# Performance work log

Hardware: AMD Instinct MI355X
Metric: run time of the kernel (lower is better)

## Reference

```python
import jax, jax.numpy as jnp
import numpy as np

B, S, D, H = 4, 2048, 1024, 16
HD = D // H

def rotate_half(x):
    x1, x2 = jnp.split(x, 2, axis=-1)
    return jnp.concatenate((-x2, x1), axis=-1)

def apply_rope(x, cos, sin):
    # x: [B,H,S,hd]; cos/sin: [S,hd] -> broadcast over B,H
    return x * cos[None, None] + rotate_half(x) * sin[None, None]

def setup_inputs() -> dict:
    key = jax.random.key(0)
    ks = jax.random.split(key, 8)
    x = jax.random.normal(ks[0], (B, S, D), dtype=jnp.float32)
    mask = jnp.triu(jnp.ones((S, S), dtype=bool), k=1)  # True = masked (causal)
    pos = jnp.arange(S, dtype=jnp.float32)[:, None]
    inv = 1.0 / (10000.0 ** (jnp.arange(0, HD, 2, dtype=jnp.float32) / HD))
    ang = pos * inv[None, :]  # [S, hd/2]
    ang = jnp.concatenate([ang, ang], axis=-1)  # [S, hd]
    rope_cos = jnp.cos(ang)
    rope_sin = jnp.sin(ang)
    scale = 1.0 / np.sqrt(D)
    Wq = jax.random.normal(ks[1], (D, D), dtype=jnp.float32) * scale
    Wk = jax.random.normal(ks[2], (D, D), dtype=jnp.float32) * scale
    Wv = jax.random.normal(ks[3], (D, D), dtype=jnp.float32) * scale
    Wo = jax.random.normal(ks[4], (D, D), dtype=jnp.float32) * scale
    z = jnp.zeros((D,), dtype=jnp.float32)
    return {"x": x, "mask": mask, "rope_cos": rope_cos, "rope_sin": rope_sin,
            "Wq": Wq, "bq": z, "Wk": Wk, "bk": z, "Wv": Wv, "bv": z, "Wo": Wo, "bo": z}

def reference(x, mask, rope_cos, rope_sin, Wq, bq, Wk, bk, Wv, bv, Wo, bo):
    b, s, d = x.shape
    def proj(W, bias):
        y = x @ W.T + bias  # torch Linear: x W^T + b
        return y.reshape(b, s, H, HD).transpose(0, 2, 1, 3)  # [B,H,S,hd]
    Q = apply_rope(proj(Wq, bq), rope_cos, rope_sin)
    K = apply_rope(proj(Wk, bk), rope_cos, rope_sin)
    V = proj(Wv, bv)
    scores = jnp.einsum('bhqd,bhkd->bhqk', Q, K) / jnp.sqrt(jnp.float32(HD))
    scores = jnp.where(mask[None, None], -jnp.inf, scores)
    attn = jax.nn.softmax(scores, axis=-1)
    ctx = jnp.einsum('bhqk,bhkd->bhqd', attn, V)
    ctx = ctx.transpose(0, 2, 1, 3).reshape(b, s, d)
    return ctx @ Wo.T + bo
```

## Files before the change

kernel.cpp:

```cpp
#include <hip/hip_runtime.h>
#include <hip/hip_bf16.h>

#define S_LEN 2048
#define D_MODEL 1024
#define NH 16
#define HDIM 64
#define B_SZ 4

typedef __attribute__((ext_vector_type(8))) short bf16x8;
typedef __attribute__((ext_vector_type(4))) float f32x4;

__device__ inline void gld16(const __hip_bfloat16* g, __hip_bfloat16* l) {
    __builtin_amdgcn_global_load_lds(
        (const __attribute__((address_space(1))) unsigned int*)g,
        (__attribute__((address_space(3))) unsigned int*)l, 16, 0, 0);
}

__device__ inline unsigned int pkbf(float a, float b) {
    float2 f; f.x = a; f.y = b;
    __hip_bfloat162 h = __float22bfloat162_rn(f);
    union { __hip_bfloat162 h; unsigned int u; } cv; cv.h = h; return cv.u;
}

__global__ __launch_bounds__(256) void f2bf4_kernel(const float4* __restrict__ in,
                                                    __hip_bfloat162* __restrict__ out,
                                                    int n4) {
    int i = blockIdx.x * 256 + threadIdx.x;
    if (i < n4) {
        float4 v = in[i];
        __hip_bfloat162 a, b;
        a.x = __float2bfloat16(v.x); a.y = __float2bfloat16(v.y);
        b.x = __float2bfloat16(v.z); b.y = __float2bfloat16(v.w);
        out[2 * i]     = a;
        out[2 * i + 1] = b;
    }
}

__global__ __launch_bounds__(256) void f2bfw_kernel(
    const float4* __restrict__ w0, const float4* __restrict__ w1,
    const float4* __restrict__ w2, const float4* __restrict__ w3,
    __hip_bfloat162* __restrict__ o0, __hip_bfloat162* __restrict__ o1,
    __hip_bfloat162* __restrict__ o2, __hip_bfloat162* __restrict__ o3) {
    const int z = blockIdx.y;
    const float4* in = (z == 0) ? w0 : (z == 1) ? w1 : (z == 2) ? w2 : w3;
    __hip_bfloat162* out = (z == 0) ? o0 : (z == 1) ? o1 : (z == 2) ? o2 : o3;
    int i = blockIdx.x * 256 + threadIdx.x;
    float4 v = in[i];
    __hip_bfloat162 a, b;
    a.x = __float2bfloat16(v.x); a.y = __float2bfloat16(v.y);
    b.x = __float2bfloat16(v.z); b.y = __float2bfloat16(v.w);
    out[2 * i]     = a;
    out[2 * i + 1] = b;
}

__device__ inline void gemm_mainloop(const __hip_bfloat16* __restrict__ X,
                                     const __hip_bfloat16* __restrict__ W,
                                     __hip_bfloat16* As, __hip_bfloat16* Bs,
                                     int m0, int n0, f32x4 acc[4][4]) {
    const int tid = threadIdx.x;
    const int wv = tid >> 6, lane = tid & 63, l15 = lane & 15, quad = lane >> 4;
    const int rw = (wv >> 1) * 64, cw = (wv & 1) * 64;
    for (int k0 = 0; k0 < D_MODEL; k0 += 32) {
        __syncthreads();
#pragma unroll
        for (int i = 0; i < 2; i++) {
            int l = tid + 256 * i;
            int row = l >> 2, c8 = (l & 3) * 8;
            gld16(&X[(size_t)(m0 + row) * D_MODEL + k0 + c8], &As[row * 32 + c8]);
            gld16(&W[(size_t)(n0 + row) * D_MODEL + k0 + c8], &Bs[row * 32 + c8]);
        }
        __syncthreads();
        bf16x8 af[4], bfr[4];
#pragma unroll
        for (int t = 0; t < 4; t++)
            af[t] = *(const bf16x8*)&As[(rw + t * 16 + l15) * 32 + quad * 8];
#pragma unroll
        for (int t = 0; t < 4; t++)
            bfr[t] = *(const bf16x8*)&Bs[(cw + t * 16 + l15) * 32 + quad * 8];
#pragma unroll
        for (int mt = 0; mt < 4; mt++)
#pragma unroll
            for (int nt = 0; nt < 4; nt++)
                acc[mt][nt] = __builtin_amdgcn_mfma_f32_16x16x32_bf16(
                    af[mt], bfr[nt], acc[mt][nt], 0, 0, 0);
    }
}

#define PT 136
__global__ __launch_bounds__(256) void qkv_kernel(
    const __hip_bfloat16* __restrict__ X,
    const __hip_bfloat16* __restrict__ W0, const __hip_bfloat16* __restrict__ W1,
    const __hip_bfloat16* __restrict__ W2,
    const float* __restrict__ b0, const float* __restrict__ b1,
    const float* __restrict__ b2,
    const float* __restrict__ rc, const float* __restrict__ rs,
    __hip_bfloat16* __restrict__ Qo, __hip_bfloat16* __restrict__ Ko,
    __hip_bfloat16* __restrict__ Vo) {
    __shared__ __hip_bfloat16 pool[64 * PT];
    __hip_bfloat16* As = pool;
    __hip_bfloat16* Bs = pool + 4096;
    const int z = blockIdx.z;
    const __hip_bfloat16* W = (z == 0) ? W0 : ((z == 1) ? W1 : W2);
    const float* bias = (z == 0) ? b0 : ((z == 1) ? b1 : b2);
    f32x4 acc[4][4];
#pragma unroll
    for (int i = 0; i < 4; i++)
#pragma unroll
        for (int j = 0; j < 4; j++) acc[i][j] = (f32x4){0.f, 0.f, 0.f, 0.f};
    const int m0 = blockIdx.x * 128, n0 = blockIdx.y * 128;
    gemm_mainloop(X, W, As, Bs, m0, n0, acc);

    const int tid = threadIdx.x;
    const int wv = tid >> 6, lane = tid & 63, l15 = lane & 15, quad = lane >> 4;
    const int rw = (wv >> 1) * 64, cw = (wv & 1) * 64;

    if (z == 2) {
        __hip_bfloat16* T = pool;
        const int b = m0 >> 11, s0l = m0 & (S_LEN - 1);
#pragma unroll
        for (int hn = 0; hn < 2; hn++) {
            __syncthreads();
            if ((wv & 1) == hn) {
#pragma unroll
                for (int mt = 0; mt < 4; mt++)
#pragma unroll
                    for (int nt = 0; nt < 4; nt++)
#pragma unroll
                        for (int r = 0; r < 4; r++) {
                            int dl = nt * 16 + l15;
                            int ml = rw + mt * 16 + quad * 4 + r;
                            T[dl * PT + ml] =
                                __float2bfloat16(acc[mt][nt][r] + bias[n0 + hn * 64 + dl]);
                        }
            }
            __syncthreads();
            const int d = tid >> 2, sc = tid & 3;
            const int h = (n0 >> 6) + hn;
            size_t gb = ((size_t)((b * NH + h) * HDIM + d)) * S_LEN + s0l + sc * 32;
#pragma unroll
            for (int j = 0; j < 4; j++) {
                bf16x8 v = *(const bf16x8*)&T[d * PT + sc * 32 + j * 8];
                *(bf16x8*)&Vo[gb + j * 8] = v;
            }
        }
    } else {
        __hip_bfloat16* dst = (z == 0) ? Qo : Ko;
        const float qs = (z == 0) ? 0.18033688011112042f : 1.0f;
#pragma unroll
        for (int mt = 0; mt < 4; mt++)
#pragma unroll
            for (int r = 0; r < 4; r++) {
                int m = m0 + rw + mt * 16 + quad * 4 + r;
                int s = m & (S_LEN - 1), b = m >> 11;
#pragma unroll
                for (int nt = 0; nt < 2; nt++) {
                    int n1 = n0 + cw + nt * 16 + l15;
                    int h = n1 >> 6, hd1 = n1 & 63;
                    float y1 = acc[mt][nt][r] + bias[n1];
                    float y2 = acc[mt][nt + 2][r] + bias[n1 + 32];
                    float c1 = rc[s * HDIM + hd1], s1 = rs[s * HDIM + hd1];
                    float c2 = rc[s * HDIM + hd1 + 32], s2 = rs[s * HDIM + hd1 + 32];
                    size_t base = (((size_t)(b * NH + h)) * S_LEN + s) * HDIM;
                    dst[base + hd1]      = __float2bfloat16((y1 * c1 - y2 * s1) * qs);
                    dst[base + hd1 + 32] = __float2bfloat16((y2 * c2 + y1 * s2) * qs);
                }
            }
    }
}

#define SWZ(r, c) (((r) << 6) + ((c) ^ (((r) & 7) << 3)))
__global__ __launch_bounds__(256) void attn_kernel(
    const __hip_bfloat16* __restrict__ Q, const __hip_bfloat16* __restrict__ K,
    const __hip_bfloat16* __restrict__ VT, __hip_bfloat16* __restrict__ CTX) {
    __shared__ __hip_bfloat16 Kl[2][64 * 64];
    __shared__ __hip_bfloat16 Vl[2][64 * 64];
    __shared__ __hip_bfloat16 Pl[2][4][16 * 64];
    const int tid = threadIdx.x;
    const int wv = tid >> 6, lane = tid & 63, l15 = lane & 15, quad = lane >> 4;
    const int bh = blockIdx.x;
    const int pr = blockIdx.y;
    const int tA = pr, tC = 31 - pr;
    const int nkb = tC + 1;
    const size_t off = (size_t)bh * S_LEN * HDIM;
    const __hip_bfloat16* Qp = Q + off;
    const __hip_bfloat16* Kp = K + off;
    const __hip_bfloat16* Vp = VT + off;
    __hip_bfloat16* PC = &Pl[0][wv][0];
    __hip_bfloat16* PA = &Pl[1][wv][0];

    const int e0 = wv * 512 + lane * 8;
    const int r0 = e0 >> 6, c80 = e0 & 63;
    const int sw0 = c80 ^ ((r0 & 7) << 3);
    const int r1 = r0 + 32;
    const int sw1 = c80 ^ ((r1 & 7) << 3);
    const __hip_bfloat16* ks0 = Kp + r0 * 64 + sw0;
    const __hip_bfloat16* ks1 = Kp + r1 * 64 + sw1;
    const __hip_bfloat16* vs0 = Vp + (size_t)r0 * S_LEN + sw0;
    const __hip_bfloat16* vs1 = Vp + (size_t)r1 * S_LEN + sw1;

    auto stage = [&](int kb, int bsel) {
        const int ko = kb * 64;
        gld16(ks0 + (size_t)ko * 64, &Kl[bsel][e0]);
        gld16(ks1 + (size_t)ko * 64, &Kl[bsel][e0 + 2048]);
        gld16(vs0 + ko, &Vl[bsel][e0]);
        gld16(vs1 + ko, &Vl[bsel][e0 + 2048]);
    };

    bf16x8 qfA[2], qfC[2];
#pragma unroll
    for (int c = 0; c < 2; c++) {
        qfA[c] = *(const bf16x8*)&Qp[(size_t)(tA * 64 + wv * 16 + l15) * HDIM + c * 32 + quad * 8];
        qfC[c] = *(const bf16x8*)&Qp[(size_t)(tC * 64 + wv * 16 + l15) * HDIM + c * 32 + quad * 8];
    }

    float lA = 0.f, lC = 0.f;
    f32x4 accA[4], accC[4];
#pragma unroll
    for (int nt = 0; nt < 4; nt++) {
        accA[nt] = (f32x4){0.f, 0.f, 0.f, 0.f};
        accC[nt] = (f32x4){0.f, 0.f, 0.f, 0.f};
    }

    const int qrel = wv * 16 + l15;

    stage(0, 0);
    __syncthreads();
    for (int kb = 0; kb < nkb; kb++) {
        const int buf = kb & 1;
        if (kb + 1 < nkb) stage(kb + 1, buf ^ 1);
        const __hip_bfloat16* Kb_ = &Kl[buf][0];
        const __hip_bfloat16* Vb_ = &Vl[buf][0];

        const bool aAct = (kb <= tA);
        unsigned int pkC[8], pkA[8];

        f32x4 saC[4], saA[4];
#pragma unroll
        for (int st = 0; st < 4; st++) {
            saC[st] = (f32x4){0.f, 0.f, 0.f, 0.f};
            saA[st] = (f32x4){0.f, 0.f, 0.f, 0.f};
        }
        __builtin_amdgcn_s_setprio(1);
        if (aAct) {
#pragma unroll
            for (int c = 0; c < 2; c++)
#pragma unroll
                for (int st = 0; st < 4; st++) {
                    bf16x8 kf = *(const bf16x8*)&Kb_[SWZ(st * 16 + l15, c * 32 + quad * 8)];
                    saC[st] = __builtin_amdgcn_mfma_f32_16x16x32_bf16(kf, qfC[c], saC[st], 0, 0, 0);
                    saA[st] = __builtin_amdgcn_mfma_f32_16x16x32_bf16(kf, qfA[c], saA[st], 0, 0, 0);
                }
        } else {
#pragma unroll
            for (int c = 0; c < 2; c++)
#pragma unroll
                for (int st = 0; st < 4; st++) {
                    bf16x8 kf = *(const bf16x8*)&Kb_[SWZ(st * 16 + l15, c * 32 + quad * 8)];
                    saC[st] = __builtin_amdgcn_mfma_f32_16x16x32_bf16(kf, qfC[c], saC[st], 0, 0, 0);
                }
        }
        __builtin_amdgcn_s_setprio(0);

        {
            float ls = 0.f;
            if (kb == tC) {
#pragma unroll
                for (int st = 0; st < 4; st++) {
                    float p[4];
#pragma unroll
                    for (int r = 0; r < 4; r++) {
                        bool msk = (st * 16 + quad * 4 + r > qrel);
                        p[r] = msk ? 0.f : __builtin_exp2f(saC[st][r]);
                        ls += p[r];
                    }
                    pkC[st * 2 + 0] = pkbf(p[0], p[1]);
                    pkC[st * 2 + 1] = pkbf(p[2], p[3]);
                }
            } else {
#pragma unroll
                for (int st = 0; st < 4; st++) {
                    float p[4];
#pragma unroll
                    for (int r = 0; r < 4; r++) {
                        p[r] = __builtin_exp2f(saC[st][r]);
                        ls += p[r];
                    }
                    pkC[st * 2 + 0] = pkbf(p[0], p[1]);
                    pkC[st * 2 + 1] = pkbf(p[2], p[3]);
                }
            }
            ls += __shfl_xor(ls, 16);
            ls += __shfl_xor(ls, 32);
            lC += ls;
#pragma unroll
            for (int st = 0; st < 4; st++) {
                uint2 w; w.x = pkC[st * 2]; w.y = pkC[st * 2 + 1];
                *(uint2*)&PC[SWZ(l15, st * 16 + quad * 4)] = w;
            }
        }
        if (aAct) {
            float ls = 0.f;
            if (kb == tA) {
#pragma unroll
                for (int st = 0; st < 4; st++) {
                    float p[4];
#pragma unroll
                    for (int r = 0; r < 4; r++) {
                        bool msk = (st * 16 + quad * 4 + r > qrel);
                        p[r] = msk ? 0.f : __builtin_exp2f(saA[st][r]);
                        ls += p[r];
                    }
                    pkA[st * 2 + 0] = pkbf(p[0], p[1]);
                    pkA[st * 2 + 1] = pkbf(p[2], p[3]);
                }
            } else {
#pragma unroll
                for (int st = 0; st < 4; st++) {
                    float p[4];
#pragma unroll
                    for (int r = 0; r < 4; r++) {
                        p[r] = __builtin_exp2f(saA[st][r]);
                        ls += p[r];
                    }
                    pkA[st * 2 + 0] = pkbf(p[0], p[1]);
                    pkA[st * 2 + 1] = pkbf(p[2], p[3]);
                }
            }
            ls += __shfl_xor(ls, 16);
            ls += __shfl_xor(ls, 32);
            lA += ls;
#pragma unroll
            for (int st = 0; st < 4; st++) {
                uint2 w; w.x = pkA[st * 2]; w.y = pkA[st * 2 + 1];
                *(uint2*)&PA[SWZ(l15, st * 16 + quad * 4)] = w;
            }
        }

        __builtin_amdgcn_s_setprio(1);
#pragma unroll
        for (int c = 0; c < 2; c++) {
            bf16x8 vf[4];
#pragma unroll
            for (int nt = 0; nt < 4; nt++)
                vf[nt] = *(const bf16x8*)&Vb_[SWZ(nt * 16 + l15, c * 32 + quad * 8)];
            {
                bf16x8 pf = *(const bf16x8*)&PC[SWZ(l15, c * 32 + quad * 8)];
#pragma unroll
                for (int nt = 0; nt < 4; nt++)
                    accC[nt] = __builtin_amdgcn_mfma_f32_16x16x32_bf16(vf[nt], pf, accC[nt], 0, 0, 0);
            }
            if (aAct) {
                bf16x8 pf = *(const bf16x8*)&PA[SWZ(l15, c * 32 + quad * 8)];
#pragma unroll
                for (int nt = 0; nt < 4; nt++)
                    accA[nt] = __builtin_amdgcn_mfma_f32_16x16x32_bf16(vf[nt], pf, accA[nt], 0, 0, 0);
            }
        }
        __builtin_amdgcn_s_setprio(0);

        __syncthreads();
    }

    const int b = bh >> 4, h = bh & 15;
    {
        const int q = tA * 64 + wv * 16 + l15;
        const float inv = 1.0f / lA;
#pragma unroll
        for (int nt = 0; nt < 4; nt++) {
            uint2 st2;
            st2.x = pkbf(accA[nt][0] * inv, accA[nt][1] * inv);
            st2.y = pkbf(accA[nt][2] * inv, accA[nt][3] * inv);
            *(uint2*)&CTX[((size_t)(b * S_LEN + q)) * D_MODEL + h * HDIM + nt * 16 + quad * 4] = st2;
        }
    }
    {
        const int q = tC * 64 + wv * 16 + l15;
        const float inv = 1.0f / lC;
#pragma unroll
        for (int nt = 0; nt < 4; nt++) {
            uint2 st2;
            st2.x = pkbf(accC[nt][0] * inv, accC[nt][1] * inv);
            st2.y = pkbf(accC[nt][2] * inv, accC[nt][3] * inv);
            *(uint2*)&CTX[((size_t)(b * S_LEN + q)) * D_MODEL + h * HDIM + nt * 16 + quad * 4] = st2;
        }
    }
}

__global__ __launch_bounds__(256) void outproj_kernel(
    const __hip_bfloat16* __restrict__ X, const __hip_bfloat16* __restrict__ W,
    const float* __restrict__ bias, float* __restrict__ OUT) {
    __shared__ __hip_bfloat16 As[128 * 32];
    __shared__ __hip_bfloat16 Bs[128 * 32];
    f32x4 acc[4][4];
#pragma unroll
    for (int i = 0; i < 4; i++)
#pragma unroll
        for (int j = 0; j < 4; j++) acc[i][j] = (f32x4){0.f, 0.f, 0.f, 0.f};
    const int m0 = blockIdx.x * 128, n0 = blockIdx.y * 128;
    gemm_mainloop(X, W, As, Bs, m0, n0, acc);
    const int tid = threadIdx.x;
    const int wv = tid >> 6, lane = tid & 63, l15 = lane & 15, quad = lane >> 4;
    const int rw = (wv >> 1) * 64, cw = (wv & 1) * 64;
#pragma unroll
    for (int mt = 0; mt < 4; mt++)
#pragma unroll
        for (int r = 0; r < 4; r++) {
            int m = m0 + rw + mt * 16 + quad * 4 + r;
#pragma unroll
            for (int nt = 0; nt < 4; nt++) {
                int n = n0 + cw + nt * 16 + l15;
                OUT[(size_t)m * D_MODEL + n] = acc[mt][nt][r] + bias[n];
            }
        }
}

extern "C" void kernel_launch(void* const* d_in, const int* in_sizes, int n_in,
                              void* d_out, int out_size, void* d_ws, size_t ws_size,
                              hipStream_t stream) {
    const float* x  = (const float*)d_in[0];
    const float* rc = (const float*)d_in[2];
    const float* rs = (const float*)d_in[3];
    const float* Wq = (const float*)d_in[4];
    const float* bq = (const float*)d_in[5];
    const float* Wk = (const float*)d_in[6];
    const float* bk = (const float*)d_in[7];
    const float* Wv = (const float*)d_in[8];
    const float* bv = (const float*)d_in[9];
    const float* Wo = (const float*)d_in[10];
    const float* bo = (const float*)d_in[11];

    char* ws = (char*)d_ws;
    __hip_bfloat16* xbf = (__hip_bfloat16*)(ws);
    __hip_bfloat16* wqb = (__hip_bfloat16*)(ws + (16u << 20));
    __hip_bfloat16* wkb = (__hip_bfloat16*)(ws + (18u << 20));
    __hip_bfloat16* wvb = (__hip_bfloat16*)(ws + (20u << 20));
    __hip_bfloat16* wob = (__hip_bfloat16*)(ws + (22u << 20));
    __hip_bfloat16* Qb  = (__hip_bfloat16*)(ws + (24u << 20));
    __hip_bfloat16* Kb  = (__hip_bfloat16*)(ws + (40u << 20));
    __hip_bfloat16* Vb  = (__hip_bfloat16*)(ws + (56u << 20));
    __hip_bfloat16* Cb  = (__hip_bfloat16*)(ws + (72u << 20));
    float* out = (float*)d_out;

    f2bf4_kernel<<<8192, 256, 0, stream>>>((const float4*)x, (__hip_bfloat162*)xbf, 2097152);
    f2bfw_kernel<<<dim3(1024, 4), 256, 0, stream>>>(
        (const float4*)Wq, (const float4*)Wk, (const float4*)Wv, (const float4*)Wo,
        (__hip_bfloat162*)wqb, (__hip_bfloat162*)wkb, (__hip_bfloat162*)wvb,
        (__hip_bfloat162*)wob);

    qkv_kernel<<<dim3(64, 8, 3), 256, 0, stream>>>(xbf, wqb, wkb, wvb, bq, bk, bv,
                                                   rc, rs, Qb, Kb, Vb);
    attn_kernel<<<dim3(64, 16), 256, 0, stream>>>(Qb, Kb, Vb, Cb);
    outproj_kernel<<<dim3(64, 8), 256, 0, stream>>>(Cb, wob, bo, out);
}
```

Measured before the change: 313.0 us.

## Stage Q/K RoPE epilogue through LDS for vectorized stores; drop setprio

The Q/K projection epilogue now writes the biased accumulators as bf16 into a shared-memory tile in two halves. Threads then read 8-wide rows, apply RoPE with vectorized cos/sin loads, and write 16-byte stores to Q/K, replacing scattered 2-byte global stores. The aim is to coalesce the epilogue's global traffic. The change also removes the s_setprio hints around the MFMA blocks in the attention kernel. It adds barriers and an extra bf16 rounding of the pre-RoPE values, which slightly changes numerics.

Result: no change. 316.0 us (+1.0%).

```diff
diff --git a/kernel.cpp b/kernel.cpp
--- a/kernel.cpp
+++ b/kernel.cpp
@@ -9,6 +9,7 @@
 
 typedef __attribute__((ext_vector_type(8))) short bf16x8;
 typedef __attribute__((ext_vector_type(4))) float f32x4;
+typedef __attribute__((ext_vector_type(8))) float f32x8;
 
 __device__ inline void gld16(const __hip_bfloat16* g, __hip_bfloat16* l) {
     __builtin_amdgcn_global_load_lds(
@@ -20,6 +21,12 @@
     float2 f; f.x = a; f.y = b;
     __hip_bfloat162 h = __float22bfloat162_rn(f);
     union { __hip_bfloat162 h; unsigned int u; } cv; cv.h = h; return cv.u;
+}
+
+__device__ inline float b2f(short u) {
+    union { unsigned int i; float f; } c;
+    c.i = ((unsigned int)(unsigned short)u) << 16;
+    return c.f;
 }
 
 __global__ __launch_bounds__(256) void f2bf4_kernel(const float4* __restrict__ in,
@@ -144,27 +151,57 @@
             }
         }
     } else {
+        __hip_bfloat16* T = pool;
         __hip_bfloat16* dst = (z == 0) ? Qo : Ko;
         const float qs = (z == 0) ? 0.18033688011112042f : 1.0f;
 #pragma unroll
-        for (int mt = 0; mt < 4; mt++)
-#pragma unroll
-            for (int r = 0; r < 4; r++) {
-                int m = m0 + rw + mt * 16 + quad * 4 + r;
-                int s = m & (S_LEN - 1), b = m >> 11;
-#pragma unroll
-                for (int nt = 0; nt < 2; nt++) {
-                    int n1 = n0 + cw + nt * 16 + l15;
-                    int h = n1 >> 6, hd1 = n1 & 63;
-                    float y1 = acc[mt][nt][r] + bias[n1];
-                    float y2 = acc[mt][nt + 2][r] + bias[n1 + 32];
-                    float c1 = rc[s * HDIM + hd1], s1 = rs[s * HDIM + hd1];
-                    float c2 = rc[s * HDIM + hd1 + 32], s2 = rs[s * HDIM + hd1 + 32];
-                    size_t base = (((size_t)(b * NH + h)) * S_LEN + s) * HDIM;
-                    dst[base + hd1]      = __float2bfloat16((y1 * c1 - y2 * s1) * qs);
-                    dst[base + hd1 + 32] = __float2bfloat16((y2 * c2 + y1 * s2) * qs);
-                }
-            }
+        for (int p = 0; p < 2; p++) {
+            __syncthreads();
+            if ((wv >> 1) == p) {
+#pragma unroll
+                for (int mt = 0; mt < 4; mt++)
+#pragma unroll
+                    for (int nt = 0; nt < 4; nt++)
+#pragma unroll
+                        for (int r = 0; r < 4; r++) {
+                            int ml = mt * 16 + quad * 4 + r;
+                            int nl = cw + nt * 16 + l15;
+                            T[ml * PT + nl] =
+                                __float2bfloat16(acc[mt][nt][r] + bias[n0 + nl]);
+                        }
+            }
+            __syncthreads();
+            const int ml = tid >> 2, ch = (tid >> 1) & 1, jh = tid & 1;
+            const int mg = m0 + p * 64 + ml;
+            const int s = mg & (S_LEN - 1), b = mg >> 11;
+            const int h = (n0 >> 6) + ch;
+            const size_t gb = (((size_t)(b * NH + h)) * S_LEN + s) * HDIM;
+#pragma unroll
+            for (int jj = 0; jj < 2; jj++) {
+                const int j = jj * 2 + jh;
+                bf16x8 ya = *(const bf16x8*)&T[ml * PT + ch * 64 + j * 8];
+                bf16x8 yb = *(const bf16x8*)&T[ml * PT + ch * 64 + j * 8 + 32];
+                f32x8 cl = *(const f32x8*)&rc[s * HDIM + j * 8];
+                f32x8 sl = *(const f32x8*)&rs[s * HDIM + j * 8];
+                f32x8 chv = *(const f32x8*)&rc[s * HDIM + j * 8 + 32];
+                f32x8 shv = *(const f32x8*)&rs[s * HDIM + j * 8 + 32];
+                float lo[8], hi[8];
+#pragma unroll
+                for (int i = 0; i < 8; i++) {
+                    float y1 = b2f(ya[i]), y2 = b2f(yb[i]);
+                    lo[i] = (y1 * cl[i] - y2 * sl[i]) * qs;
+                    hi[i] = (y2 * chv[i] + y1 * shv[i]) * qs;
+                }
+                union { unsigned int u[4]; bf16x8 v; } plo, phi;
+#pragma unroll
+                for (int i = 0; i < 4; i++) {
+                    plo.u[i] = pkbf(lo[2 * i], lo[2 * i + 1]);
+                    phi.u[i] = pkbf(hi[2 * i], hi[2 * i + 1]);
+                }
+                *(bf16x8*)&dst[gb + j * 8]      = plo.v;
+                *(bf16x8*)&dst[gb + j * 8 + 32] = phi.v;
+            }
+        }
     }
 }
 
@@ -240,7 +277,6 @@
             saC[st] = (f32x4){0.f, 0.f, 0.f, 0.f};
             saA[st] = (f32x4){0.f, 0.f, 0.f, 0.f};
         }
-        __builtin_amdgcn_s_setprio(1);
         if (aAct) {
 #pragma unroll
             for (int c = 0; c < 2; c++)
@@ -259,7 +295,6 @@
                     saC[st] = __builtin_amdgcn_mfma_f32_16x16x32_bf16(kf, qfC[c], saC[st], 0, 0, 0);
                 }
         }
-        __builtin_amdgcn_s_setprio(0);
 
         {
             float ls = 0.f;
@@ -336,7 +371,6 @@
             }
         }
 
-        __builtin_amdgcn_s_setprio(1);
 #pragma unroll
         for (int c = 0; c < 2; c++) {
             bf16x8 vf[4];
@@ -356,7 +390,6 @@
                     accA[nt] = __builtin_amdgcn_mfma_f32_16x16x32_bf16(vf[nt], pf, accA[nt], 0, 0, 0);
             }
         }
-        __builtin_amdgcn_s_setprio(0);
 
         __syncthreads();
     }
```

## Double-buffer GEMM mainloop LDS tiles and drop setprio in attention

Applied to the files above, without the earlier changes.

The shared GEMM mainloop used by the QKV and output projections now double-buffers its A and B LDS tiles. Each iteration issues the async global-to-LDS loads for the next k-slice before the MFMAs on the current slice, so one barrier per iteration replaces two and load latency can overlap compute. This doubles LDS per block (the QKV pool grows to 16384 elements), which may lower occupancy. Separately, the s_setprio raise/lower around the attention MFMA sections is removed.

New measurement: 302.6 us. 1.03x faster.

```diff
diff --git a/kernel.cpp b/kernel.cpp
--- a/kernel.cpp
+++ b/kernel.cpp
@@ -60,29 +60,42 @@
     const int tid = threadIdx.x;
     const int wv = tid >> 6, lane = tid & 63, l15 = lane & 15, quad = lane >> 4;
     const int rw = (wv >> 1) * 64, cw = (wv & 1) * 64;
+    const int r0 = tid >> 2, c0 = (tid & 3) * 8;
+    const int r1 = (tid + 256) >> 2, c1 = ((tid + 256) & 3) * 8;
+    const __hip_bfloat16* xa0 = &X[(size_t)(m0 + r0) * D_MODEL + c0];
+    const __hip_bfloat16* xa1 = &X[(size_t)(m0 + r1) * D_MODEL + c1];
+    const __hip_bfloat16* wa0 = &W[(size_t)(n0 + r0) * D_MODEL + c0];
+    const __hip_bfloat16* wa1 = &W[(size_t)(n0 + r1) * D_MODEL + c1];
+    const int la0 = r0 * 32 + c0, la1 = r1 * 32 + c1;
+
+    gld16(xa0, &As[la0]); gld16(xa1, &As[la1]);
+    gld16(wa0, &Bs[la0]); gld16(wa1, &Bs[la1]);
+    __syncthreads();
     for (int k0 = 0; k0 < D_MODEL; k0 += 32) {
-        __syncthreads();
-#pragma unroll
-        for (int i = 0; i < 2; i++) {
-            int l = tid + 256 * i;
-            int row = l >> 2, c8 = (l & 3) * 8;
-            gld16(&X[(size_t)(m0 + row) * D_MODEL + k0 + c8], &As[row * 32 + c8]);
-            gld16(&W[(size_t)(n0 + row) * D_MODEL + k0 + c8], &Bs[row * 32 + c8]);
-        }
-        __syncthreads();
+        const int buf = (k0 >> 5) & 1;
+        if (k0 + 32 < D_MODEL) {
+            const int o = (buf ^ 1) * 4096;
+            gld16(xa0 + k0 + 32, &As[o + la0]);
+            gld16(xa1 + k0 + 32, &As[o + la1]);
+            gld16(wa0 + k0 + 32, &Bs[o + la0]);
+            gld16(wa1 + k0 + 32, &Bs[o + la1]);
+        }
+        const __hip_bfloat16* Ab = &As[buf * 4096];
+        const __hip_bfloat16* Bb = &Bs[buf * 4096];
         bf16x8 af[4], bfr[4];
 #pragma unroll
         for (int t = 0; t < 4; t++)
-            af[t] = *(const bf16x8*)&As[(rw + t * 16 + l15) * 32 + quad * 8];
+            af[t] = *(const bf16x8*)&Ab[(rw + t * 16 + l15) * 32 + quad * 8];
 #pragma unroll
         for (int t = 0; t < 4; t++)
-            bfr[t] = *(const bf16x8*)&Bs[(cw + t * 16 + l15) * 32 + quad * 8];
+            bfr[t] = *(const bf16x8*)&Bb[(cw + t * 16 + l15) * 32 + quad * 8];
 #pragma unroll
         for (int mt = 0; mt < 4; mt++)
 #pragma unroll
             for (int nt = 0; nt < 4; nt++)
                 acc[mt][nt] = __builtin_amdgcn_mfma_f32_16x16x32_bf16(
                     af[mt], bfr[nt], acc[mt][nt], 0, 0, 0);
+        __syncthreads();
     }
 }
 
@@ -96,9 +109,9 @@
     const float* __restrict__ rc, const float* __restrict__ rs,
     __hip_bfloat16* __restrict__ Qo, __hip_bfloat16* __restrict__ Ko,
     __hip_bfloat16* __restrict__ Vo) {
-    __shared__ __hip_bfloat16 pool[64 * PT];
+    __shared__ __hip_bfloat16 pool[16384];
     __hip_bfloat16* As = pool;
-    __hip_bfloat16* Bs = pool + 4096;
+    __hip_bfloat16* Bs = pool + 8192;
     const int z = blockIdx.z;
     const __hip_bfloat16* W = (z == 0) ? W0 : ((z == 1) ? W1 : W2);
     const float* bias = (z == 0) ? b0 : ((z == 1) ? b1 : b2);
@@ -240,7 +253,6 @@
             saC[st] = (f32x4){0.f, 0.f, 0.f, 0.f};
             saA[st] = (f32x4){0.f, 0.f, 0.f, 0.f};
         }
-        __builtin_amdgcn_s_setprio(1);
         if (aAct) {
 #pragma unroll
             for (int c = 0; c < 2; c++)
@@ -259,7 +271,6 @@
                     saC[st] = __builtin_amdgcn_mfma_f32_16x16x32_bf16(kf, qfC[c], saC[st], 0, 0, 0);
                 }
         }
-        __builtin_amdgcn_s_setprio(0);
 
         {
             float ls = 0.f;
@@ -336,7 +347,6 @@
             }
         }
 
-        __builtin_amdgcn_s_setprio(1);
 #pragma unroll
         for (int c = 0; c < 2; c++) {
             bf16x8 vf[4];
@@ -356,7 +366,6 @@
                     accA[nt] = __builtin_amdgcn_mfma_f32_16x16x32_bf16(vf[nt], pf, accA[nt], 0, 0, 0);
             }
         }
-        __builtin_amdgcn_s_setprio(0);
 
         __syncthreads();
     }
@@ -389,8 +398,8 @@
 __global__ __launch_bounds__(256) void outproj_kernel(
     const __hip_bfloat16* __restrict__ X, const __hip_bfloat16* __restrict__ W,
     const float* __restrict__ bias, float* __restrict__ OUT) {
-    __shared__ __hip_bfloat16 As[128 * 32];
-    __shared__ __hip_bfloat16 Bs[128 * 32];
+    __shared__ __hip_bfloat16 As[2 * 4096];
+    __shared__ __hip_bfloat16 Bs[2 * 4096];
     f32x4 acc[4][4];
 #pragma unroll
     for (int i = 0; i < 4; i++)
```

## Double-buffer GEMM mainloop with BK=64 and XOR-swizzled LDS layout

Applied to the files above, without the earlier changes.

Rewrites the shared projection GEMM mainloop to use a K tile of 64 with two LDS buffers. The next tile is prefetched via global_load_lds while the current one feeds the MFMAs, which drops one barrier per iteration. An XOR swizzle on the 16-byte column chunks is meant to avoid LDS bank conflicts. It also sets launch_bounds occupancy hints on the GEMM kernels and removes the setprio calls in the attention kernel, at the cost of 64KB of LDS per block, which may limit occupancy.

New measurement: 302.4 us. 3.4% less time.

```diff
diff --git a/kernel.cpp b/kernel.cpp
--- a/kernel.cpp
+++ b/kernel.cpp
@@ -60,34 +60,53 @@
     const int tid = threadIdx.x;
     const int wv = tid >> 6, lane = tid & 63, l15 = lane & 15, quad = lane >> 4;
     const int rw = (wv >> 1) * 64, cw = (wv & 1) * 64;
-    for (int k0 = 0; k0 < D_MODEL; k0 += 32) {
+    const int row_s = tid >> 3;
+    const int csw = ((tid & 7) ^ (row_s & 7)) * 8;
+    const __hip_bfloat16* xsrc = X + (size_t)(m0 + row_s) * D_MODEL + csw;
+    const __hip_bfloat16* wsrc = W + (size_t)(n0 + row_s) * D_MODEL + csw;
+    const int ld = tid * 8;
+
+    auto stage = [&](int k0, int bsel) {
+#pragma unroll
+        for (int i = 0; i < 4; i++) {
+            gld16(xsrc + (size_t)(i * 32) * D_MODEL + k0,
+                  &As[bsel * 8192 + i * 2048 + ld]);
+            gld16(wsrc + (size_t)(i * 32) * D_MODEL + k0,
+                  &Bs[bsel * 8192 + i * 2048 + ld]);
+        }
+    };
+
+    stage(0, 0);
+    __syncthreads();
+    for (int kt = 0; kt < 16; kt++) {
+        const int buf = kt & 1;
+        if (kt + 1 < 16) stage((kt + 1) * 64, buf ^ 1);
+        const __hip_bfloat16* Ab = &As[buf * 8192];
+        const __hip_bfloat16* Bb = &Bs[buf * 8192];
+#pragma unroll
+        for (int kc = 0; kc < 2; kc++) {
+            bf16x8 af[4], bfr[4];
+#pragma unroll
+            for (int t = 0; t < 4; t++)
+                af[t] = *(const bf16x8*)&Ab[(rw + t * 16 + l15) * 64 +
+                                            (((kc * 4 + quad) ^ (l15 & 7)) * 8)];
+#pragma unroll
+            for (int t = 0; t < 4; t++)
+                bfr[t] = *(const bf16x8*)&Bb[(cw + t * 16 + l15) * 64 +
+                                             (((kc * 4 + quad) ^ (l15 & 7)) * 8)];
+#pragma unroll
+            for (int mt = 0; mt < 4; mt++)
+#pragma unroll
+                for (int nt = 0; nt < 4; nt++)
+                    acc[mt][nt] = __builtin_amdgcn_mfma_f32_16x16x32_bf16(
+                        af[mt], bfr[nt], acc[mt][nt], 0, 0, 0);
+        }
         __syncthreads();
-#pragma unroll
-        for (int i = 0; i < 2; i++) {
-            int l = tid + 256 * i;
-            int row = l >> 2, c8 = (l & 3) * 8;
-            gld16(&X[(size_t)(m0 + row) * D_MODEL + k0 + c8], &As[row * 32 + c8]);
-            gld16(&W[(size_t)(n0 + row) * D_MODEL + k0 + c8], &Bs[row * 32 + c8]);
-        }
-        __syncthreads();
-        bf16x8 af[4], bfr[4];
-#pragma unroll
-        for (int t = 0; t < 4; t++)
-            af[t] = *(const bf16x8*)&As[(rw + t * 16 + l15) * 32 + quad * 8];
-#pragma unroll
-        for (int t = 0; t < 4; t++)
-            bfr[t] = *(const bf16x8*)&Bs[(cw + t * 16 + l15) * 32 + quad * 8];
-#pragma unroll
-        for (int mt = 0; mt < 4; mt++)
-#pragma unroll
-            for (int nt = 0; nt < 4; nt++)
-                acc[mt][nt] = __builtin_amdgcn_mfma_f32_16x16x32_bf16(
-                    af[mt], bfr[nt], acc[mt][nt], 0, 0, 0);
     }
 }
 
 #define PT 136
-__global__ __launch_bounds__(256) void qkv_kernel(
+__global__ __launch_bounds__(256, 2) void qkv_kernel(
     const __hip_bfloat16* __restrict__ X,
     const __hip_bfloat16* __restrict__ W0, const __hip_bfloat16* __restrict__ W1,
     const __hip_bfloat16* __restrict__ W2,
@@ -96,9 +115,9 @@
     const float* __restrict__ rc, const float* __restrict__ rs,
     __hip_bfloat16* __restrict__ Qo, __hip_bfloat16* __restrict__ Ko,
     __hip_bfloat16* __restrict__ Vo) {
-    __shared__ __hip_bfloat16 pool[64 * PT];
+    __shared__ __hip_bfloat16 pool[32768];
     __hip_bfloat16* As = pool;
-    __hip_bfloat16* Bs = pool + 4096;
+    __hip_bfloat16* Bs = pool + 16384;
     const int z = blockIdx.z;
     const __hip_bfloat16* W = (z == 0) ? W0 : ((z == 1) ? W1 : W2);
     const float* bias = (z == 0) ? b0 : ((z == 1) ? b1 : b2);
@@ -240,7 +259,6 @@
             saC[st] = (f32x4){0.f, 0.f, 0.f, 0.f};
             saA[st] = (f32x4){0.f, 0.f, 0.f, 0.f};
         }
-        __builtin_amdgcn_s_setprio(1);
         if (aAct) {
 #pragma unroll
             for (int c = 0; c < 2; c++)
@@ -259,7 +277,6 @@
                     saC[st] = __builtin_amdgcn_mfma_f32_16x16x32_bf16(kf, qfC[c], saC[st], 0, 0, 0);
                 }
         }
-        __builtin_amdgcn_s_setprio(0);
 
         {
             float ls = 0.f;
@@ -336,7 +353,6 @@
             }
         }
 
-        __builtin_amdgcn_s_setprio(1);
 #pragma unroll
         for (int c = 0; c < 2; c++) {
             bf16x8 vf[4];
@@ -356,7 +372,6 @@
                     accA[nt] = __builtin_amdgcn_mfma_f32_16x16x32_bf16(vf[nt], pf, accA[nt], 0, 0, 0);
             }
         }
-        __builtin_amdgcn_s_setprio(0);
 
         __syncthreads();
     }
@@ -386,11 +401,11 @@
     }
 }
 
-__global__ __launch_bounds__(256) void outproj_kernel(
+__global__ __launch_bounds__(256, 2) void outproj_kernel(
     const __hip_bfloat16* __restrict__ X, const __hip_bfloat16* __restrict__ W,
     const float* __restrict__ bias, float* __restrict__ OUT) {
-    __shared__ __hip_bfloat16 As[128 * 32];
-    __shared__ __hip_bfloat16 Bs[128 * 32];
+    __shared__ __hip_bfloat16 As[2 * 8192];
+    __shared__ __hip_bfloat16 Bs[2 * 8192];
     f32x4 acc[4][4];
 #pragma unroll
     for (int i = 0; i < 4; i++)
```
